# Kernel optimization log

Hardware: AMD Instinct MI355X
Metric: run time of the kernel (lower is better)

The kernel has to match this reference:

```python
import jax, jax.numpy as jnp
import numpy as np

N = 30000
N_CONTEXT = 32
IN_FEAT = 256
HIDDEN = 128
ALPHA = 0.2
NEG_INF = -9e15


def setup_inputs() -> dict:
    key = jax.random.key(0)
    k1, k2, k3, k4, k5, k6, k7 = jax.random.split(key, 7)
    h_i = jax.random.normal(k1, (N, IN_FEAT), dtype=jnp.float32)
    idx = jax.random.randint(k2, (N, N_CONTEXT), 0, N)
    pad = jax.random.uniform(k3, (N, N_CONTEXT)) < 0.1
    context_indices = jnp.where(pad, -1, idx)
    s_in = 1.0 / np.sqrt(IN_FEAT)
    s_h = 1.0 / np.sqrt(2 * HIDDEN)
    W_i = jax.random.uniform(k4, (IN_FEAT, HIDDEN), minval=-s_in, maxval=s_in, dtype=jnp.float32)
    W_j = jax.random.uniform(k5, (IN_FEAT, HIDDEN), minval=-s_in, maxval=s_in, dtype=jnp.float32)
    a_w = jax.random.uniform(k6, (2 * HIDDEN,), minval=-s_h, maxval=s_h, dtype=jnp.float32)
    a_b = jax.random.uniform(k7, (), minval=-s_h, maxval=s_h, dtype=jnp.float32)
    return {"h_i": h_i, "context_indices": context_indices,
            "W_i": W_i, "W_j": W_j, "a_w": a_w, "a_b": a_b}


def reference(h_i, context_indices, W_i, W_j, a_w, a_b):
    # Pad with a zero-feature row; index -1 hits the last row (same as torch cat trick).
    h_padded = jnp.concatenate([h_i, jnp.zeros((1, h_i.shape[1]), h_i.dtype)], axis=0)
    h_j = h_padded[context_indices]                       # [N, C, F] gather
    Wh_i = h_i @ W_i                                      # [N, H]
    Wh_j = jnp.einsum('ncf,fh->nch', h_j, W_j)            # [N, C, H]
    # attention_layer(cat(Wh_i, Wh_j)) split into two dot products + bias
    scores = (Wh_i @ a_w[:HIDDEN])[:, None] + Wh_j @ a_w[HIDDEN:] + a_b  # [N, C]
    scores = jnp.where(scores >= 0, scores, ALPHA * scores)              # leaky relu
    scores = jnp.where(context_indices >= 0, scores, NEG_INF)
    attn = jax.nn.softmax(scores, axis=1)                 # [N, C]
    h_prime = jnp.einsum('nc,nch->nh', attn, Wh_j)        # [N, H]
    return h_prime
```

## Files before the change

kernel.cpp:

```cpp
#include <hip/hip_runtime.h>

#define NN   30000
#define NCTX 32
#define FIN  256
#define HID  128

typedef short short8 __attribute__((ext_vector_type(8)));
typedef float f32x4  __attribute__((ext_vector_type(4)));

__device__ __forceinline__ unsigned short f2b(float x) {
    union { float f; unsigned u; } v; v.f = x;
    unsigned r = v.u + 0x7FFFu + ((v.u >> 16) & 1u);
    return (unsigned short)(r >> 16);
}
__device__ __forceinline__ unsigned short f2b_trunc(float x) {
    union { float f; unsigned u; } v; v.f = x;
    return (unsigned short)(v.u >> 16);
}
__device__ __forceinline__ float b2f(unsigned short u) {
    union { unsigned u; float f; } v; v.u = ((unsigned)u) << 16;
    return v.f;
}

__global__ __launch_bounds__(64) void k_pack(const float* __restrict__ Wj,
                                             const float* __restrict__ Wi,
                                             const float* __restrict__ aw,
                                             short8* __restrict__ whi,
                                             short8* __restrict__ wlo,
                                             float* __restrict__ vi) {
    const int b = blockIdx.x;
    const int l = threadIdx.x;
    if (b >= 64) {
        const int fi = l >> 4;
        const int q  = l & 15;
        const int f  = (b - 64) * 4 + fi;
        const float4 w0 = *(const float4*)(Wi + (long)f * HID + q * 8);
        const float4 w1 = *(const float4*)(Wi + (long)f * HID + q * 8 + 4);
        const float4 a0 = *(const float4*)(aw + q * 8);
        const float4 a1 = *(const float4*)(aw + q * 8 + 4);
        float s = w0.x * a0.x + w0.y * a0.y + w0.z * a0.z + w0.w * a0.w
                + w1.x * a1.x + w1.y * a1.y + w1.z * a1.z + w1.w * a1.w;
        s += __shfl_xor(s, 1); s += __shfl_xor(s, 2);
        s += __shfl_xor(s, 4); s += __shfl_xor(s, 8);
        if (q == 0) vi[f] = s;
        return;
    }
    const int s = b >> 3, t = b & 7;
    const int kbase = s * 32 + (l >> 4) * 8;
    const int c = t * 16 + (l & 15);
    short8 hi, lo;
    #pragma unroll
    for (int j = 0; j < 8; ++j) {
        const float w = Wj[(long)(kbase + j) * HID + c];
        const unsigned short h = f2b_trunc(w);
        hi[j] = (short)h;
        lo[j] = (short)f2b(w - b2f(h));
    }
    whi[b * 64 + l] = hi;
    wlo[b * 64 + l] = lo;
}

__global__ __launch_bounds__(256) void k_gemm(const float* __restrict__ hin,
                                              const short8* __restrict__ whi,
                                              const short8* __restrict__ wlo,
                                              const float* __restrict__ vi,
                                              const float* __restrict__ aw,
                                              const float* __restrict__ ab,
                                              unsigned short* __restrict__ Wh,
                                              float* __restrict__ sib,
                                              float* __restrict__ sjv) {
    const int tid  = threadIdx.x;
    const int l    = tid & 63;
    const int wave = blockIdx.x * 4 + (tid >> 6);
    if (wave >= NN / 16) return;
    const long rowbase = (long)wave * 16;
    const int r  = l & 15;
    const int kg = l >> 4;

    const float* hrow = hin + (rowbase + r) * FIN + kg * 8;
    const float* vip  = vi + kg * 8;

    f32x4 acc[8];
    #pragma unroll
    for (int t = 0; t < 8; ++t) acc[t] = (f32x4){0.f, 0.f, 0.f, 0.f};
    float si = 0.f;

    #pragma unroll
    for (int s = 0; s < 8; ++s) {
        short8 BH[8], BL[8];
        #pragma unroll
        for (int t = 0; t < 8; ++t) {
            BH[t] = whi[(s * 8 + t) * 64 + l];
            BL[t] = wlo[(s * 8 + t) * 64 + l];
        }
        const float4 ha = *(const float4*)(hrow + s * 32);
        const float4 hb = *(const float4*)(hrow + s * 32 + 4);
        const float4 va = *(const float4*)(vip + s * 32);
        const float4 vb = *(const float4*)(vip + s * 32 + 4);
        const float hv[8] = {ha.x, ha.y, ha.z, ha.w, hb.x, hb.y, hb.z, hb.w};
        const float vv[8] = {va.x, va.y, va.z, va.w, vb.x, vb.y, vb.z, vb.w};
        short8 ahi, alo;
        #pragma unroll
        for (int j = 0; j < 8; ++j) {
            si += hv[j] * vv[j];
            const unsigned short hb16 = f2b_trunc(hv[j]);
            ahi[j] = (short)hb16;
            alo[j] = (short)f2b(hv[j] - b2f(hb16));
        }
        #pragma unroll
        for (int t = 0; t < 8; ++t) {
            acc[t] = __builtin_amdgcn_mfma_f32_16x16x32_bf16(ahi, BH[t], acc[t], 0, 0, 0);
            acc[t] = __builtin_amdgcn_mfma_f32_16x16x32_bf16(alo, BH[t], acc[t], 0, 0, 0);
            acc[t] = __builtin_amdgcn_mfma_f32_16x16x32_bf16(ahi, BL[t], acc[t], 0, 0, 0);
        }
    }

    si += __shfl_xor(si, 16);
    si += __shfl_xor(si, 32);
    if (l < 16) sib[rowbase + l] = si + ab[0];

    float aw2v[8];
    #pragma unroll
    for (int t = 0; t < 8; ++t) aw2v[t] = aw[HID + t * 16 + r];
    #pragma unroll
    for (int j = 0; j < 4; ++j) {
        float p = 0.f;
        #pragma unroll
        for (int t = 0; t < 8; ++t) p += acc[t][j] * aw2v[t];
        p += __shfl_xor(p, 1); p += __shfl_xor(p, 2);
        p += __shfl_xor(p, 4); p += __shfl_xor(p, 8);
        if (r == 0) sjv[rowbase + kg * 4 + j] = p;
    }

    #pragma unroll
    for (int j = 0; j < 4; ++j) {
        const long rr = rowbase + kg * 4 + j;
        #pragma unroll
        for (int t = 0; t < 8; ++t)
            Wh[rr * HID + t * 16 + r] = f2b(acc[t][j]);
    }
}

__global__ __launch_bounds__(256) void k_attn(const int* __restrict__ ctx,
                                              const unsigned short* __restrict__ Wh,
                                              const float* __restrict__ sib,
                                              const float* __restrict__ sjv,
                                              float* __restrict__ out) {
    const int lane = threadIdx.x & 63;
    const long n = (long)blockIdx.x * 4 + (threadIdx.x >> 6);
    const int c = lane & 31;
    const int idx = ctx[n * NCTX + c];
    const int icl = (idx >= 0) ? idx : 0;
    float s;
    if (idx >= 0) {
        s = sib[n] + sjv[icl];
        s = (s >= 0.f) ? s : 0.2f * s;
    } else {
        s = -9e15f;
    }
    float mx = s;
    #pragma unroll
    for (int m = 16; m >= 1; m >>= 1) mx = fmaxf(mx, __shfl_xor(mx, m));
    const float e = __expf(s - mx);
    float sum = e;
    #pragma unroll
    for (int m = 16; m >= 1; m >>= 1) sum += __shfl_xor(sum, m);
    const float at = (idx >= 0) ? e / sum : 0.f;

    const int q  = lane >> 4;
    const int cl = lane & 15;

    float a0 = 0.f, a1 = 0.f, a2 = 0.f, a3 = 0.f, a4 = 0.f, a5 = 0.f, a6 = 0.f, a7 = 0.f;
    #pragma unroll
    for (int it = 0; it < 8; ++it) {
        const int   src = it * 4 + q;
        const float w   = __shfl(at, src);
        const int   ic  = __shfl(icl, src);
        const uint4 pv  = *(const uint4*)(Wh + (long)ic * HID + cl * 8);
        a0 += w * b2f((unsigned short)(pv.x & 0xFFFFu));
        a1 += w * b2f((unsigned short)(pv.x >> 16));
        a2 += w * b2f((unsigned short)(pv.y & 0xFFFFu));
        a3 += w * b2f((unsigned short)(pv.y >> 16));
        a4 += w * b2f((unsigned short)(pv.z & 0xFFFFu));
        a5 += w * b2f((unsigned short)(pv.z >> 16));
        a6 += w * b2f((unsigned short)(pv.w & 0xFFFFu));
        a7 += w * b2f((unsigned short)(pv.w >> 16));
    }
    #pragma unroll
    for (int m = 16; m <= 32; m <<= 1) {
        a0 += __shfl_xor(a0, m); a1 += __shfl_xor(a1, m);
        a2 += __shfl_xor(a2, m); a3 += __shfl_xor(a3, m);
        a4 += __shfl_xor(a4, m); a5 += __shfl_xor(a5, m);
        a6 += __shfl_xor(a6, m); a7 += __shfl_xor(a7, m);
    }
    if (lane < 16) {
        float4* op = (float4*)(out + n * HID + cl * 8);
        op[0] = (float4){a0, a1, a2, a3};
        op[1] = (float4){a4, a5, a6, a7};
    }
}

extern "C" void kernel_launch(void* const* d_in, const int* in_sizes, int n_in,
                              void* d_out, int out_size, void* d_ws, size_t ws_size,
                              hipStream_t stream) {
    const float* h_i = (const float*)d_in[0];
    const int*   ctx = (const int*)d_in[1];
    const float* W_i = (const float*)d_in[2];
    const float* W_j = (const float*)d_in[3];
    const float* a_w = (const float*)d_in[4];
    const float* a_b = (const float*)d_in[5];
    float* out = (float*)d_out;

    char* ws = (char*)d_ws;
    unsigned short* Wh = (unsigned short*)ws;
    float* sib = (float*)(ws + 7680000);
    float* sjv = (float*)(ws + 7800000);
    float* vi  = (float*)(ws + 7920000);
    short8* whi = (short8*)(ws + 7921024);
    short8* wlo = (short8*)(ws + 7986560);

    k_pack<<<128, 64, 0, stream>>>(W_j, W_i, a_w, whi, wlo, vi);
    k_gemm<<<(NN / 16 + 3) / 4, 256, 0, stream>>>(h_i, whi, wlo, vi, a_w, a_b, Wh, sib, sjv);
    k_attn<<<NN / 4, 256, 0, stream>>>(ctx, Wh, sib, sjv, out);
}
```

Baseline: 52.15 us.

## Process two nodes per wave in attention kernel and batch gathers

Previously the upper 32 lanes of each wave duplicated the score and softmax work for the same node. The attention kernel now gives each 32-lane half of a wave its own node, which halves the grid. All 16 gathered Wh row loads per lane are issued up front, before any accumulation, so more memory requests are in flight at once. The cost is higher register use per lane for the buffered loads and weights, which may lower occupancy.

```diff
diff --git a/kernel.cpp b/kernel.cpp
--- a/kernel.cpp
+++ b/kernel.cpp
@@ -147,8 +147,11 @@
                                               const float* __restrict__ sjv,
                                               float* __restrict__ out) {
     const int lane = threadIdx.x & 63;
-    const long n = (long)blockIdx.x * 4 + (threadIdx.x >> 6);
-    const int c = lane & 31;
+    const long n0 = ((long)blockIdx.x * 4 + (threadIdx.x >> 6)) * 2;
+    const int half = lane >> 5;
+    const int c    = lane & 31;
+    const long n   = n0 + half;
+
     const int idx = ctx[n * NCTX + c];
     const int icl = (idx >= 0) ? idx : 0;
     float s;
@@ -167,36 +170,62 @@
     for (int m = 16; m >= 1; m >>= 1) sum += __shfl_xor(sum, m);
     const float at = (idx >= 0) ? e / sum : 0.f;
 
-    const int q  = lane >> 4;
+    const int rq = lane >> 4;
     const int cl = lane & 15;
 
-    float a0 = 0.f, a1 = 0.f, a2 = 0.f, a3 = 0.f, a4 = 0.f, a5 = 0.f, a6 = 0.f, a7 = 0.f;
-    #pragma unroll
-    for (int it = 0; it < 8; ++it) {
-        const int   src = it * 4 + q;
-        const float w   = __shfl(at, src);
-        const int   ic  = __shfl(icl, src);
-        const uint4 pv  = *(const uint4*)(Wh + (long)ic * HID + cl * 8);
-        a0 += w * b2f((unsigned short)(pv.x & 0xFFFFu));
-        a1 += w * b2f((unsigned short)(pv.x >> 16));
-        a2 += w * b2f((unsigned short)(pv.y & 0xFFFFu));
-        a3 += w * b2f((unsigned short)(pv.y >> 16));
-        a4 += w * b2f((unsigned short)(pv.z & 0xFFFFu));
-        a5 += w * b2f((unsigned short)(pv.z >> 16));
-        a6 += w * b2f((unsigned short)(pv.w & 0xFFFFu));
-        a7 += w * b2f((unsigned short)(pv.w >> 16));
-    }
-    #pragma unroll
-    for (int m = 16; m <= 32; m <<= 1) {
-        a0 += __shfl_xor(a0, m); a1 += __shfl_xor(a1, m);
-        a2 += __shfl_xor(a2, m); a3 += __shfl_xor(a3, m);
-        a4 += __shfl_xor(a4, m); a5 += __shfl_xor(a5, m);
-        a6 += __shfl_xor(a6, m); a7 += __shfl_xor(a7, m);
+    float w0[8], w1[8];
+    int   i0[8], i1[8];
+    #pragma unroll
+    for (int i = 0; i < 8; ++i) {
+        w0[i] = __shfl(at,  i * 4 + rq);
+        i0[i] = __shfl(icl, i * 4 + rq);
+        w1[i] = __shfl(at,  32 + i * 4 + rq);
+        i1[i] = __shfl(icl, 32 + i * 4 + rq);
+    }
+    uint4 L0[8], L1[8];
+    #pragma unroll
+    for (int i = 0; i < 8; ++i)
+        L0[i] = *(const uint4*)(Wh + (long)i0[i] * HID + cl * 8);
+    #pragma unroll
+    for (int i = 0; i < 8; ++i)
+        L1[i] = *(const uint4*)(Wh + (long)i1[i] * HID + cl * 8);
+
+    float a[8] = {0.f,0.f,0.f,0.f,0.f,0.f,0.f,0.f};
+    float b[8] = {0.f,0.f,0.f,0.f,0.f,0.f,0.f,0.f};
+    #pragma unroll
+    for (int i = 0; i < 8; ++i) {
+        const uint4 p0 = L0[i]; const float w = w0[i];
+        a[0] += w * b2f((unsigned short)(p0.x & 0xFFFFu));
+        a[1] += w * b2f((unsigned short)(p0.x >> 16));
+        a[2] += w * b2f((unsigned short)(p0.y & 0xFFFFu));
+        a[3] += w * b2f((unsigned short)(p0.y >> 16));
+        a[4] += w * b2f((unsigned short)(p0.z & 0xFFFFu));
+        a[5] += w * b2f((unsigned short)(p0.z >> 16));
+        a[6] += w * b2f((unsigned short)(p0.w & 0xFFFFu));
+        a[7] += w * b2f((unsigned short)(p0.w >> 16));
+        const uint4 p1 = L1[i]; const float v = w1[i];
+        b[0] += v * b2f((unsigned short)(p1.x & 0xFFFFu));
+        b[1] += v * b2f((unsigned short)(p1.x >> 16));
+        b[2] += v * b2f((unsigned short)(p1.y & 0xFFFFu));
+        b[3] += v * b2f((unsigned short)(p1.y >> 16));
+        b[4] += v * b2f((unsigned short)(p1.z & 0xFFFFu));
+        b[5] += v * b2f((unsigned short)(p1.z >> 16));
+        b[6] += v * b2f((unsigned short)(p1.w & 0xFFFFu));
+        b[7] += v * b2f((unsigned short)(p1.w >> 16));
+    }
+    #pragma unroll
+    for (int i = 0; i < 8; ++i) {
+        a[i] += __shfl_xor(a[i], 16); a[i] += __shfl_xor(a[i], 32);
+        b[i] += __shfl_xor(b[i], 16); b[i] += __shfl_xor(b[i], 32);
     }
     if (lane < 16) {
-        float4* op = (float4*)(out + n * HID + cl * 8);
-        op[0] = (float4){a0, a1, a2, a3};
-        op[1] = (float4){a4, a5, a6, a7};
+        float4* op = (float4*)(out + n0 * HID + cl * 8);
+        op[0] = (float4){a[0], a[1], a[2], a[3]};
+        op[1] = (float4){a[4], a[5], a[6], a[7]};
+    } else if (lane < 32) {
+        float4* op = (float4*)(out + (n0 + 1) * HID + cl * 8);
+        op[0] = (float4){b[0], b[1], b[2], b[3]};
+        op[1] = (float4){b[4], b[5], b[6], b[7]};
     }
 }
 
@@ -221,5 +250,5 @@
 
     k_pack<<<128, 64, 0, stream>>>(W_j, W_i, a_w, whi, wlo, vi);
     k_gemm<<<(NN / 16 + 3) / 4, 256, 0, stream>>>(h_i, whi, wlo, vi, a_w, a_b, Wh, sib, sjv);
-    k_attn<<<NN / 4, 256, 0, stream>>>(ctx, Wh, sib, sjv, out);
-}
+    k_attn<<<NN / 8, 256, 0, stream>>>(ctx, Wh, sib, sjv, out);
+}
```

Result: slower. 54.22 us (+4.0%).
